# Kernel optimization log

Hardware: AMD Instinct MI355X
Metric: run time of the kernel (lower is better)

The kernel has to match this reference:

```python
import jax, jax.numpy as jnp
import numpy as np

N, E, D, ED, G = 50000, 600000, 128, 32, 64
NEG_SLOPE = 0.2

def layer_norm(x, g, b, eps=1e-5):
    mu = jnp.mean(x, axis=-1, keepdims=True)
    var = jnp.var(x, axis=-1, keepdims=True)
    return (x - mu) * jax.lax.rsqrt(var + eps) * g + b

def eagat(x, src, dst, edge_attr, W, a_src, a_dst, We, a_e, bias):
    # GATConv with edge features, heads=1; messages flow src -> dst
    xl = x @ W                               # [N, D]
    ee = edge_attr @ We                      # [E, D]
    al_s = xl @ a_src                        # [N]
    al_d = xl @ a_dst                        # [N]
    e = jax.nn.leaky_relu(al_s[src] + al_d[dst] + ee @ a_e, NEG_SLOPE)  # [E]
    # segment softmax over incoming edges of each dst node
    m = jax.ops.segment_max(e, dst, num_segments=N)
    ex = jnp.exp(e - m[dst])
    s = jax.ops.segment_sum(ex, dst, num_segments=N)
    alpha = ex / (s[dst] + 1e-16)            # [E]
    out = jax.ops.segment_sum(xl[src] * alpha[:, None], dst, num_segments=N)
    return out + bias

def setup_inputs() -> dict:
    key = jax.random.key(0)
    ks = jax.random.split(key, 24)
    p = lambda k, shp, sc=0.1: jax.random.normal(k, shp, dtype=jnp.float32) * sc
    inp = {
        "x": jax.random.normal(ks[0], (N, D), dtype=jnp.float32),
        "edge_attr": jax.random.normal(ks[1], (E, ED), dtype=jnp.float32),
        "W1": p(ks[2], (D, D)), "as1": p(ks[3], (D,)), "ad1": p(ks[4], (D,)),
        "We1": p(ks[5], (ED, D)), "ae1": p(ks[6], (D,)), "b1": jnp.zeros((D,), jnp.float32),
        "g1": jnp.ones((D,), jnp.float32), "be1": jnp.zeros((D,), jnp.float32),
        "W2": p(ks[7], (D, D)), "as2": p(ks[8], (D,)), "ad2": p(ks[9], (D,)),
        "We2": p(ks[10], (ED, D)), "ae2": p(ks[11], (D,)), "b2": jnp.zeros((D,), jnp.float32),
        "g2": jnp.ones((D,), jnp.float32), "be2": jnp.zeros((D,), jnp.float32),
        "Wl": p(ks[12], (D, D)), "bl": jnp.zeros((D,), jnp.float32),
        "gl": jnp.ones((D,), jnp.float32), "bel": jnp.zeros((D,), jnp.float32),
        "edge_index": jax.random.randint(ks[13], (2, E), 0, N, dtype=jnp.int64),
        "batch": jnp.sort(jax.random.randint(ks[14], (N,), 0, G, dtype=jnp.int64)),
    }
    return inp

def reference(x, edge_attr, W1, as1, ad1, We1, ae1, b1, g1, be1,
              W2, as2, ad2, We2, ae2, b2, g2, be2, Wl, bl, gl, bel,
              edge_index, batch):
    src, dst = edge_index[0], edge_index[1]
    x1 = eagat(x, src, dst, edge_attr, W1, as1, ad1, We1, ae1, b1)
    x2 = layer_norm(x1, g1, be1)
    x3 = eagat(x2, src, dst, edge_attr, W2, as2, ad2, We2, ae2, b2)
    x4 = layer_norm(x3, g2, be2)
    # global mean pool over graphs
    sums = jax.ops.segment_sum(x4, batch, num_segments=G)          # [G, D]
    cnt = jax.ops.segment_sum(jnp.ones((x4.shape[0],), x4.dtype), batch, num_segments=G)
    pooled = sums / jnp.maximum(cnt, 1.0)[:, None]
    out = jax.nn.relu(layer_norm(pooled @ Wl + bl, gl, bel))
    return out
```

## Files before the change

### kernel.cpp

```cpp
#include <hip/hip_runtime.h>
#include <math.h>


typedef __attribute__((ext_vector_type(8))) short bf16x8;
typedef __attribute__((ext_vector_type(4))) float f32x4;

static __device__ __forceinline__ unsigned short f2bf(float f) {
    unsigned u = __float_as_uint(f);
    unsigned r = (u + 0x7fff + ((u >> 16) & 1)) >> 16;
    return (unsigned short)r;
}
static __device__ __forceinline__ float bf2f_lo(unsigned u) { return __uint_as_float(u << 16); }
static __device__ __forceinline__ float bf2f_hi(unsigned u) { return __uint_as_float(u & 0xffff0000u); }

__global__ __launch_bounds__(256) void prep_weights(
    const float* __restrict__ W1, const float* __restrict__ W2,
    const float* __restrict__ We1, const float* __restrict__ ae1,
    const float* __restrict__ We2, const float* __restrict__ ae2,
    unsigned short* __restrict__ W1bT, unsigned short* __restrict__ W2bT,
    float* __restrict__ wa, int4* __restrict__ counts4, int nc4,
    int4* __restrict__ pooled4, int np4, int zc)
{
    int b = blockIdx.x, t = threadIdx.x;
    if (b < 64) {
        int i = b * 256 + t;
        int k = i >> 7, n = i & 127;
        W1bT[n * 128 + k] = f2bf(W1[i]);
        W2bT[n * 128 + k] = f2bf(W2[i]);
    } else if (b == 64) {
        if (t < 64) {
            const float* We = (t < 32) ? We1 : We2;
            const float* ae = (t < 32) ? ae1 : ae2;
            int r = t & 31;
            float s = 0.f;
            for (int c = 0; c < 128; c++) s += We[r*128 + c] * ae[c];
            wa[t] = s;
        }
    } else if (b < 65 + zc) {
        int i = (b - 65) * 256 + t;
        if (i < nc4) counts4[i] = (int4){0, 0, 0, 0};
    } else {
        int i = (b - 65 - zc) * 256 + t;
        if (i < np4) pooled4[i] = (int4){0, 0, 0, 0};
    }
}

__global__ __launch_bounds__(256) void edge_dots_count(
    const float* __restrict__ ea, const float* __restrict__ wa,
    const int* __restrict__ srcv, const int* __restrict__ dstv,
    int* __restrict__ counts, int2* __restrict__ payload, int E)
{
    int j = blockIdx.x * 256 + threadIdx.x;
    if (j >= E) return;
    const float4* e4 = (const float4*)(ea + (size_t)j * 32);
    float s1 = 0.f, s2 = 0.f;
#pragma unroll
    for (int i = 0; i < 8; i++) {
        float4 v = e4[i];
        float4 w1 = ((const float4*)wa)[i];
        float4 w2 = ((const float4*)(wa + 32))[i];
        s1 += v.x*w1.x + v.y*w1.y + v.z*w1.z + v.w*w1.w;
        s2 += v.x*w2.x + v.y*w2.y + v.z*w2.z + v.w*w2.w;
    }
    int dst = dstv[j];
    int r = atomicAdd(&counts[dst], 1);
    if (r < 64) {
        unsigned pe = ((unsigned)f2bf(s1) << 16) | (unsigned)f2bf(s2);
        int2 v;
        v.x = srcv[j];
        v.y = (int)pe;
        payload[((size_t)dst << 6) + r] = v;
    }
}

template<bool BF16IN>
__global__ __launch_bounds__(256) void gemm_mfma(
    const void* __restrict__ Xv, const unsigned short* __restrict__ WbT,
    const float* __restrict__ asrc, const float* __restrict__ adst,
    unsigned short* __restrict__ XLb, float* __restrict__ als, float* __restrict__ ald,
    int nrows)
{
    int t = threadIdx.x;
    int wave = t >> 6;
    int lane = t & 63;
    int l = lane & 15, q = lane >> 4;
    int row0 = blockIdx.x * 64 + wave * 16;

    int arow = row0 + l;
    bool avalid = arow < nrows;

    f32x4 acc[8];
#pragma unroll
    for (int c = 0; c < 8; c++) acc[c] = (f32x4){0.f, 0.f, 0.f, 0.f};

#pragma unroll
    for (int kt = 0; kt < 4; kt++) {
        bf16x8 afrag;
        if (avalid) {
            if constexpr (BF16IN) {
                const unsigned short* xrow = (const unsigned short*)Xv + (size_t)arow * 128 + q * 8;
                afrag = *(const bf16x8*)(xrow + kt * 32);
            } else {
                const float* xrow = (const float*)Xv + (size_t)arow * 128 + q * 8;
                float4 v0 = *(const float4*)(xrow + kt * 32);
                float4 v1 = *(const float4*)(xrow + kt * 32 + 4);
                afrag[0] = (short)f2bf(v0.x); afrag[1] = (short)f2bf(v0.y);
                afrag[2] = (short)f2bf(v0.z); afrag[3] = (short)f2bf(v0.w);
                afrag[4] = (short)f2bf(v1.x); afrag[5] = (short)f2bf(v1.y);
                afrag[6] = (short)f2bf(v1.z); afrag[7] = (short)f2bf(v1.w);
            }
        } else {
#pragma unroll
            for (int j = 0; j < 8; j++) afrag[j] = 0;
        }
#pragma unroll
        for (int c = 0; c < 8; c++) {
            bf16x8 bfrag = *(const bf16x8*)(WbT + (((c * 16 + l) << 7) + kt * 32 + q * 8));
            acc[c] = __builtin_amdgcn_mfma_f32_16x16x32_bf16(afrag, bfrag, acc[c], 0, 0, 0);
        }
    }

    float as_[8], ad_[8];
#pragma unroll
    for (int c = 0; c < 8; c++) { as_[c] = asrc[c * 16 + l]; ad_[c] = adst[c * 16 + l]; }

#pragma unroll
    for (int r = 0; r < 4; r++) {
        int row = row0 + q * 4 + r;
        bool valid = row < nrows;
        float ps = 0.f, pd = 0.f;
#pragma unroll
        for (int c = 0; c < 8; c++) {
            float v = acc[c][r];
            if (valid) XLb[(size_t)row * 128 + c * 16 + l] = f2bf(v);
            ps += v * as_[c]; pd += v * ad_[c];
        }
#pragma unroll
        for (int o = 8; o >= 1; o >>= 1) { ps += __shfl_xor(ps, o); pd += __shfl_xor(pd, o); }
        if (l == 0 && valid) { als[row] = ps; ald[row] = pd; }
    }
}

template<int EOFF>
__global__ __launch_bounds__(256) void aggregate_ln(
    const unsigned short* __restrict__ XLb, const int2* __restrict__ payload,
    const int* __restrict__ counts,
    const float* __restrict__ als, const float* __restrict__ ald,
    const float* __restrict__ bias, const float* __restrict__ gamma, const float* __restrict__ beta,
    unsigned short* __restrict__ XoutB, int N)
{
    int node = blockIdx.x * 4 + (threadIdx.x >> 6);
    if (node >= N) return;
    int lane = threadIdx.x & 63;
    int deg = counts[node];
    if (deg > 64) deg = 64;
    float ald_n = ald[node];

    const unsigned* rows = (const unsigned*)XLb;

    float w_mine = 0.f;
    int   s_mine = 0;
    if (lane < deg) {
        int2 pv = payload[((size_t)node << 6) + lane];
        s_mine = pv.x;
        unsigned ue = (unsigned)pv.y;
        float ed = (EOFF == 1) ? bf2f_hi(ue) : bf2f_lo(ue);
        float e = ed + als[s_mine] + ald_n;
        e = (e >= 0.f) ? e : 0.2f * e;
        w_mine = __expf(fminf(e, 60.f));
    }

    float ssum = w_mine;
#pragma unroll
    for (int o = 32; o >= 1; o >>= 1) ssum += __shfl_xor(ssum, o);

    float acc0 = 0.f, acc1 = 0.f;
    int j = 0;
    for (; j + 8 <= deg; j += 8) {
        int s0=__shfl(s_mine,j),   s1=__shfl(s_mine,j+1), s2=__shfl(s_mine,j+2), s3=__shfl(s_mine,j+3);
        int s4=__shfl(s_mine,j+4), s5=__shfl(s_mine,j+5), s6=__shfl(s_mine,j+6), s7=__shfl(s_mine,j+7);
        unsigned u0 = rows[((size_t)s0 << 6) + lane];
        unsigned u1 = rows[((size_t)s1 << 6) + lane];
        unsigned u2 = rows[((size_t)s2 << 6) + lane];
        unsigned u3 = rows[((size_t)s3 << 6) + lane];
        unsigned u4 = rows[((size_t)s4 << 6) + lane];
        unsigned u5 = rows[((size_t)s5 << 6) + lane];
        unsigned u6 = rows[((size_t)s6 << 6) + lane];
        unsigned u7 = rows[((size_t)s7 << 6) + lane];
        float w0=__shfl(w_mine,j),   w1=__shfl(w_mine,j+1), w2=__shfl(w_mine,j+2), w3=__shfl(w_mine,j+3);
        float w4=__shfl(w_mine,j+4), w5=__shfl(w_mine,j+5), w6=__shfl(w_mine,j+6), w7=__shfl(w_mine,j+7);
        acc0 += w0*bf2f_lo(u0); acc1 += w0*bf2f_hi(u0);
        acc0 += w1*bf2f_lo(u1); acc1 += w1*bf2f_hi(u1);
        acc0 += w2*bf2f_lo(u2); acc1 += w2*bf2f_hi(u2);
        acc0 += w3*bf2f_lo(u3); acc1 += w3*bf2f_hi(u3);
        acc0 += w4*bf2f_lo(u4); acc1 += w4*bf2f_hi(u4);
        acc0 += w5*bf2f_lo(u5); acc1 += w5*bf2f_hi(u5);
        acc0 += w6*bf2f_lo(u6); acc1 += w6*bf2f_hi(u6);
        acc0 += w7*bf2f_lo(u7); acc1 += w7*bf2f_hi(u7);
    }
    for (; j + 4 <= deg; j += 4) {
        int s0=__shfl(s_mine,j), s1=__shfl(s_mine,j+1), s2=__shfl(s_mine,j+2), s3=__shfl(s_mine,j+3);
        unsigned u0 = rows[((size_t)s0 << 6) + lane];
        unsigned u1 = rows[((size_t)s1 << 6) + lane];
        unsigned u2 = rows[((size_t)s2 << 6) + lane];
        unsigned u3 = rows[((size_t)s3 << 6) + lane];
        float w0=__shfl(w_mine,j), w1=__shfl(w_mine,j+1), w2=__shfl(w_mine,j+2), w3=__shfl(w_mine,j+3);
        acc0 += w0*bf2f_lo(u0); acc1 += w0*bf2f_hi(u0);
        acc0 += w1*bf2f_lo(u1); acc1 += w1*bf2f_hi(u1);
        acc0 += w2*bf2f_lo(u2); acc1 += w2*bf2f_hi(u2);
        acc0 += w3*bf2f_lo(u3); acc1 += w3*bf2f_hi(u3);
    }
    for (; j < deg; j++) {
        int s0 = __shfl(s_mine, j);
        float w0 = __shfl(w_mine, j);
        unsigned u0 = rows[((size_t)s0 << 6) + lane];
        acc0 += w0*bf2f_lo(u0); acc1 += w0*bf2f_hi(u0);
    }

    float2 bi = *(const float2*)(bias + 2 * lane);
    float inv = 1.f / (ssum + 1e-16f);
    float y0 = acc0 * inv + bi.x;
    float y1 = acc1 * inv + bi.y;

    float s = y0 + y1;
#pragma unroll
    for (int o = 32; o >= 1; o >>= 1) s += __shfl_xor(s, o);
    float mean = s * (1.f / 128.f);
    float d0 = y0 - mean, d1 = y1 - mean;
    float v = d0 * d0 + d1 * d1;
#pragma unroll
    for (int o = 32; o >= 1; o >>= 1) v += __shfl_xor(v, o);
    float r = rsqrtf(v * (1.f / 128.f) + 1e-5f);
    float2 ga = *(const float2*)(gamma + 2 * lane);
    float2 be = *(const float2*)(beta  + 2 * lane);
    float o0 = d0 * r * ga.x + be.x;
    float o1 = d1 * r * ga.y + be.y;
    unsigned packed = (unsigned)f2bf(o0) | ((unsigned)f2bf(o1) << 16);
    ((unsigned*)XoutB)[((size_t)node << 6) + lane] = packed;
}

__global__ __launch_bounds__(64) void pool_partial(
    const unsigned* __restrict__ XAb4, const int* __restrict__ batch,
    float* __restrict__ pooled, int n)
{
    int chunk0 = blockIdx.x * 64;
    if (chunk0 >= n) return;
    int t = threadIdx.x;
    int end = min(chunk0 + 64, n);
    float a0 = 0.f, a1 = 0.f;
    int gcur = batch[chunk0];
    for (int r = chunk0; r < end; r++) {
        int g = batch[r];
        if (g != gcur) {
            atomicAdd(&pooled[gcur * 128 + 2 * t],     a0);
            atomicAdd(&pooled[gcur * 128 + 2 * t + 1], a1);
            a0 = 0.f; a1 = 0.f; gcur = g;
        }
        unsigned u = XAb4[((size_t)r << 6) + t];
        a0 += bf2f_lo(u); a1 += bf2f_hi(u);
    }
    atomicAdd(&pooled[gcur * 128 + 2 * t],     a0);
    atomicAdd(&pooled[gcur * 128 + 2 * t + 1], a1);
}

__global__ __launch_bounds__(128) void pool_head(
    const float* __restrict__ pooled, const int* __restrict__ batch,
    const float* __restrict__ Wl, const float* __restrict__ bl,
    const float* __restrict__ gl, const float* __restrict__ bel,
    float* __restrict__ out, int n)
{
    int g = blockIdx.x, t = threadIdx.x;
    int lo = 0, hi = n;
    while (lo < hi) { int mid = (lo + hi) >> 1; if (batch[mid] < g) lo = mid + 1; else hi = mid; }
    int s = lo;
    hi = n;
    while (lo < hi) { int mid = (lo + hi) >> 1; if (batch[mid] < g + 1) lo = mid + 1; else hi = mid; }
    float cntf = (float)(lo - s);

    __shared__ float ps[128];
    __shared__ float red[128];
    ps[t] = pooled[g * 128 + t] / fmaxf(cntf, 1.f);
    __syncthreads();

    float y = bl[t];
    for (int k = 0; k < 128; k++) y += ps[k] * Wl[k * 128 + t];

    red[t] = y; __syncthreads();
#pragma unroll
    for (int o = 64; o >= 1; o >>= 1) { if (t < o) red[t] += red[t + o]; __syncthreads(); }
    float mean = red[0] * (1.f / 128.f); __syncthreads();
    float d = y - mean;
    red[t] = d * d; __syncthreads();
#pragma unroll
    for (int o = 64; o >= 1; o >>= 1) { if (t < o) red[t] += red[t + o]; __syncthreads(); }
    float var = red[0] * (1.f / 128.f);
    float z = d * rsqrtf(var + 1e-5f) * gl[t] + bel[t];
    out[g * 128 + t] = fmaxf(z, 0.f);
}


extern "C" void kernel_launch(void* const* d_in, const int* in_sizes, int n_in,
                              void* d_out, int out_size, void* d_ws, size_t ws_size,
                              hipStream_t stream)
{
    const float* x    = (const float*)d_in[0];
    const float* ea   = (const float*)d_in[1];
    const float* W1   = (const float*)d_in[2];
    const float* as1  = (const float*)d_in[3];
    const float* ad1  = (const float*)d_in[4];
    const float* We1  = (const float*)d_in[5];
    const float* ae1  = (const float*)d_in[6];
    const float* b1   = (const float*)d_in[7];
    const float* g1   = (const float*)d_in[8];
    const float* be1  = (const float*)d_in[9];
    const float* W2   = (const float*)d_in[10];
    const float* as2  = (const float*)d_in[11];
    const float* ad2  = (const float*)d_in[12];
    const float* We2  = (const float*)d_in[13];
    const float* ae2  = (const float*)d_in[14];
    const float* b2   = (const float*)d_in[15];
    const float* g2   = (const float*)d_in[16];
    const float* be2  = (const float*)d_in[17];
    const float* Wlin = (const float*)d_in[18];
    const float* bl   = (const float*)d_in[19];
    const float* gl   = (const float*)d_in[20];
    const float* bel  = (const float*)d_in[21];
    const int*   ei   = (const int*)d_in[22];
    const int*   batch= (const int*)d_in[23];
    float* out = (float*)d_out;

    int N = in_sizes[0] / 128;
    int E = in_sizes[1] / 32;
    int G = out_size / 128;
    const int* srcv = ei;
    const int* dstv = ei + E;

    char* wsb = (char*)d_ws;
    size_t off = 0;
    auto alloc = [&](size_t bytes) -> void* {
        void* p = wsb + off;
        off += (bytes + 15) & ~(size_t)15;
        return p;
    };
    unsigned short* XLb  = (unsigned short*)alloc((size_t)N * 128 * 2);
    unsigned short* XAb  = (unsigned short*)alloc((size_t)N * 128 * 2);
    unsigned short* W1bT = (unsigned short*)alloc(16384 * 2);
    unsigned short* W2bT = (unsigned short*)alloc(16384 * 2);
    int2*  payload= (int2*)alloc((size_t)N * 64 * 8);
    float* als    = (float*)alloc((size_t)N * 4);
    float* ald    = (float*)alloc((size_t)N * 4);
    float* wa     = (float*)alloc(64 * 4);
    float* pooled = (float*)alloc((size_t)G * 128 * 4);
    int*   counts = (int*)alloc((size_t)N * 4);

    int egrid = (E + 255) / 256;
    int mgrid = (N + 63) / 64;
    int agrid = (N + 3) / 4;
    int pgrid = (N + 63) / 64;

    int nc4 = N / 4 + (N % 4 != 0);
    int np4 = (G * 128) / 4;
    int zc = (nc4 + 255) / 256;
    int zp = (np4 + 255) / 256;
    prep_weights<<<65 + zc + zp, 256, 0, stream>>>(
        W1, W2, We1, ae1, We2, ae2, W1bT, W2bT, wa,
        (int4*)counts, nc4, (int4*)pooled, np4, zc);

    edge_dots_count<<<egrid, 256, 0, stream>>>(ea, wa, srcv, dstv, counts, payload, E);

    gemm_mfma<false><<<mgrid, 256, 0, stream>>>(x, W1bT, as1, ad1, XLb, als, ald, N);
    aggregate_ln<1><<<agrid, 256, 0, stream>>>(XLb, payload, counts, als, ald, b1, g1, be1, XAb, N);

    gemm_mfma<true><<<mgrid, 256, 0, stream>>>(XAb, W2bT, as2, ad2, XLb, als, ald, N);
    aggregate_ln<2><<<agrid, 256, 0, stream>>>(XLb, payload, counts, als, ald, b2, g2, be2, XAb, N);

    pool_partial<<<pgrid, 64, 0, stream>>>((const unsigned*)XAb, batch, pooled, N);
    pool_head<<<G, 128, 0, stream>>>(pooled, batch, Wlin, bl, gl, bel, out, N);
}
```

Measured before the change: 341.6 us.

## Stage GEMM output through LDS, reorder edge loads, shuffle-reduce pool head

The GEMM epilogue now packs bf16 results into a shared-memory tile and writes each row with 16-byte coalesced stores, replacing scattered 2-byte global stores. The edge kernel issues the index loads and the atomic before the attribute loads, and keeps all eight float4 loads in flight so memory latency overlaps. The pool_partial chunk size is halved to give more blocks, and pool_head replaces its tree reductions, which synchronised at every step, with wave shuffles. These changes are independent of one another; the LDS staging costs one extra block barrier and some shared memory per GEMM block.

```diff
diff --git a/kernel.cpp b/kernel.cpp
--- a/kernel.cpp
+++ b/kernel.cpp
@@ -52,24 +52,29 @@
 {
     int j = blockIdx.x * 256 + threadIdx.x;
     if (j >= E) return;
+    int dst = dstv[j];
+    int src = srcv[j];
+    int r = atomicAdd(&counts[dst], 1);
+
     const float4* e4 = (const float4*)(ea + (size_t)j * 32);
+    float4 v[8];
+#pragma unroll
+    for (int i = 0; i < 8; i++) v[i] = e4[i];
+
     float s1 = 0.f, s2 = 0.f;
 #pragma unroll
     for (int i = 0; i < 8; i++) {
-        float4 v = e4[i];
         float4 w1 = ((const float4*)wa)[i];
         float4 w2 = ((const float4*)(wa + 32))[i];
-        s1 += v.x*w1.x + v.y*w1.y + v.z*w1.z + v.w*w1.w;
-        s2 += v.x*w2.x + v.y*w2.y + v.z*w2.z + v.w*w2.w;
-    }
-    int dst = dstv[j];
-    int r = atomicAdd(&counts[dst], 1);
+        s1 += v[i].x*w1.x + v[i].y*w1.y + v[i].z*w1.z + v[i].w*w1.w;
+        s2 += v[i].x*w2.x + v[i].y*w2.y + v[i].z*w2.z + v[i].w*w2.w;
+    }
     if (r < 64) {
         unsigned pe = ((unsigned)f2bf(s1) << 16) | (unsigned)f2bf(s2);
-        int2 v;
-        v.x = srcv[j];
-        v.y = (int)pe;
-        payload[((size_t)dst << 6) + r] = v;
+        int2 pv;
+        pv.x = src;
+        pv.y = (int)pe;
+        payload[((size_t)dst << 6) + r] = pv;
     }
 }
 
@@ -80,6 +85,7 @@
     unsigned short* __restrict__ XLb, float* __restrict__ als, float* __restrict__ ald,
     int nrows)
 {
+    __shared__ unsigned short tile[64][136];
     int t = threadIdx.x;
     int wave = t >> 6;
     int lane = t & 63;
@@ -132,12 +138,35 @@
 #pragma unroll
         for (int c = 0; c < 8; c++) {
             float v = acc[c][r];
-            if (valid) XLb[(size_t)row * 128 + c * 16 + l] = f2bf(v);
             ps += v * as_[c]; pd += v * ad_[c];
         }
 #pragma unroll
         for (int o = 8; o >= 1; o >>= 1) { ps += __shfl_xor(ps, o); pd += __shfl_xor(pd, o); }
         if (l == 0 && valid) { als[row] = ps; ald[row] = pd; }
+    }
+
+#pragma unroll
+    for (int c = 0; c < 8; c++) {
+#pragma unroll
+        for (int r = 0; r < 4; r++) {
+            unsigned u = (unsigned)f2bf(acc[c][r]);
+            unsigned up = (unsigned)__shfl_xor((int)u, 1);
+            if (!(lane & 1)) {
+                *(unsigned*)&tile[wave * 16 + q * 4 + r][c * 16 + l] = u | (up << 16);
+            }
+        }
+    }
+    __syncthreads();
+
+    int base = blockIdx.x * 64;
+#pragma unroll
+    for (int it = 0; it < 4; it++) {
+        int row = it * 16 + (t >> 4);
+        int seg = t & 15;
+        if (base + row < nrows) {
+            bf16x8 vv = *(const bf16x8*)&tile[row][seg * 8];
+            *(bf16x8*)(XLb + (size_t)(base + row) * 128 + seg * 8) = vv;
+        }
     }
 }
 
@@ -243,10 +272,10 @@
     const unsigned* __restrict__ XAb4, const int* __restrict__ batch,
     float* __restrict__ pooled, int n)
 {
-    int chunk0 = blockIdx.x * 64;
+    int chunk0 = blockIdx.x * 32;
     if (chunk0 >= n) return;
     int t = threadIdx.x;
-    int end = min(chunk0 + 64, n);
+    int end = min(chunk0 + 32, n);
     float a0 = 0.f, a1 = 0.f;
     int gcur = batch[chunk0];
     for (int r = chunk0; r < end; r++) {
@@ -272,28 +301,33 @@
     int g = blockIdx.x, t = threadIdx.x;
     int lo = 0, hi = n;
     while (lo < hi) { int mid = (lo + hi) >> 1; if (batch[mid] < g) lo = mid + 1; else hi = mid; }
-    int s = lo;
+    int s0 = lo;
     hi = n;
     while (lo < hi) { int mid = (lo + hi) >> 1; if (batch[mid] < g + 1) lo = mid + 1; else hi = mid; }
-    float cntf = (float)(lo - s);
+    float cntf = (float)(lo - s0);
 
     __shared__ float ps[128];
-    __shared__ float red[128];
+    __shared__ float xr[4];
     ps[t] = pooled[g * 128 + t] / fmaxf(cntf, 1.f);
     __syncthreads();
 
     float y = bl[t];
+#pragma unroll 4
     for (int k = 0; k < 128; k++) y += ps[k] * Wl[k * 128 + t];
 
-    red[t] = y; __syncthreads();
-#pragma unroll
-    for (int o = 64; o >= 1; o >>= 1) { if (t < o) red[t] += red[t + o]; __syncthreads(); }
-    float mean = red[0] * (1.f / 128.f); __syncthreads();
+    float s = y;
+#pragma unroll
+    for (int o = 32; o >= 1; o >>= 1) s += __shfl_xor(s, o);
+    if ((t & 63) == 0) xr[t >> 6] = s;
+    __syncthreads();
+    float mean = (xr[0] + xr[1]) * (1.f / 128.f);
     float d = y - mean;
-    red[t] = d * d; __syncthreads();
-#pragma unroll
-    for (int o = 64; o >= 1; o >>= 1) { if (t < o) red[t] += red[t + o]; __syncthreads(); }
-    float var = red[0] * (1.f / 128.f);
+    float v = d * d;
+#pragma unroll
+    for (int o = 32; o >= 1; o >>= 1) v += __shfl_xor(v, o);
+    if ((t & 63) == 0) xr[2 + (t >> 6)] = v;
+    __syncthreads();
+    float var = (xr[2] + xr[3]) * (1.f / 128.f);
     float z = d * rsqrtf(var + 1e-5f) * gl[t] + bel[t];
     out[g * 128 + t] = fmaxf(z, 0.f);
 }
@@ -356,7 +390,7 @@
     int egrid = (E + 255) / 256;
     int mgrid = (N + 63) / 64;
     int agrid = (N + 3) / 4;
-    int pgrid = (N + 63) / 64;
+    int pgrid = (N + 31) / 32;
 
     int nc4 = N / 4 + (N % 4 != 0);
     int np4 = (G * 128) / 4;
```

Result: no change. 342.4 us (+0.2%).
